# Kernel tuning notes

Measured on AMD Instinct MI355X. Metric: run time of the kernel, lower is better.

## Reference

```python
import jax, jax.numpy as jnp
import numpy as np

N_NODES = 50000
N_EDGES = 800000
D_IN = 64
D_OUT = 64


def setup_inputs() -> dict:
    key = jax.random.key(0)
    ks = jax.random.split(key, 5)
    feat = jax.random.normal(ks[0], (N_NODES, D_IN), dtype=jnp.float32)
    src = jax.random.randint(ks[1], (N_EDGES,), 0, N_NODES, dtype=jnp.int64)
    dst = jax.random.randint(ks[2], (N_EDGES,), 0, N_NODES, dtype=jnp.int64)
    # Xavier-uniform-ish scale for weights
    lim = float(np.sqrt(6.0 / (D_IN + D_OUT)) * np.sqrt(2.0))
    W_neigh = jax.random.uniform(ks[3], (D_OUT, D_IN), dtype=jnp.float32, minval=-lim, maxval=lim)
    W_self = jax.random.uniform(ks[4], (D_OUT, D_IN), dtype=jnp.float32, minval=-lim, maxval=lim)
    b_self = jnp.zeros((D_OUT,), dtype=jnp.float32)
    return {"feat": feat, "src": src, "dst": dst,
            "W_neigh": W_neigh, "W_self": W_self, "b_self": b_self}


def reference(feat, src, dst, W_neigh, W_self, b_self):
    # srcdata = fc_neigh(feat_src)  -> [N, D_OUT]
    srcdata = feat @ W_neigh.T
    # A_div.T @ srcdata == mean of transformed source feats over in-edges per dst.
    # deg[j] = A.sum(0)[j]; column scaling by 1/deg then transpose-SpMM.
    agg = jax.ops.segment_sum(srcdata[src], dst, num_segments=N_NODES)  # [N, D_OUT]
    deg = jax.ops.segment_sum(jnp.ones_like(dst, dtype=srcdata.dtype), dst,
                              num_segments=N_NODES)  # [N]
    # Zero-degree columns stay zero in the sparse product (no stored nonzeros).
    dstdata = jnp.where(deg[:, None] > 0, agg / jnp.maximum(deg, 1.0)[:, None], 0.0)
    # rst = fc_self(feat_dst) + dstdata ; feat_dst = feat[:N_dst] = feat (square A)
    return feat @ W_self.T + b_self + dstdata
```

## Files before the change

kernel.cpp:

```cpp
#include <hip/hip_runtime.h>

#define N_NODES 50000
#define N_EDGES 800000
#define D 64
#define RB 128
#define NBUCK 391
#define NFEATBLK 3125
#define GN 64
#define NCHUNK 196
#define CHUNK 4096
#define SUBCAP 40
#define SCAP 3072
#define ALD 68

typedef __attribute__((ext_vector_type(8))) __bf16 bf16x8;
typedef __attribute__((ext_vector_type(4))) float f32x4;
typedef __attribute__((ext_vector_type(2))) float f32x2;

__device__ inline unsigned f2bf(float f) {
    unsigned b = __builtin_bit_cast(unsigned, f);
    b += 0x7fffu + ((b >> 16) & 1u);
    return b >> 16;
}

__device__ inline void acc16(float* acc, uint4 v) {
    f32x2 a;
    a = __builtin_amdgcn_cvt_pk_f32_fp8((int)v.x, false); acc[0]  += a.x; acc[1]  += a.y;
    a = __builtin_amdgcn_cvt_pk_f32_fp8((int)v.x, true);  acc[2]  += a.x; acc[3]  += a.y;
    a = __builtin_amdgcn_cvt_pk_f32_fp8((int)v.y, false); acc[4]  += a.x; acc[5]  += a.y;
    a = __builtin_amdgcn_cvt_pk_f32_fp8((int)v.y, true);  acc[6]  += a.x; acc[7]  += a.y;
    a = __builtin_amdgcn_cvt_pk_f32_fp8((int)v.z, false); acc[8]  += a.x; acc[9]  += a.y;
    a = __builtin_amdgcn_cvt_pk_f32_fp8((int)v.z, true);  acc[10] += a.x; acc[11] += a.y;
    a = __builtin_amdgcn_cvt_pk_f32_fp8((int)v.w, false); acc[12] += a.x; acc[13] += a.y;
    a = __builtin_amdgcn_cvt_pk_f32_fp8((int)v.w, true);  acc[14] += a.x; acc[15] += a.y;
}

__global__ __launch_bounds__(256) void prep_scatter_kernel(
        const float* __restrict__ feat, const float* __restrict__ Wn, const float* __restrict__ Ws,
        const int* __restrict__ src, const int* __restrict__ dst,
        unsigned* __restrict__ fq,
        unsigned short* __restrict__ wnb, unsigned short* __restrict__ wsb,
        unsigned int* __restrict__ ebuf, unsigned char* __restrict__ cntArr) {
    __shared__ int cntB[NBUCK];
    int b = blockIdx.x;
    int t = threadIdx.x;
    if (b < NCHUNK) {
        for (int i = t; i < NBUCK; i += 256) cntB[i] = 0;
        __syncthreads();
        int e0 = b * CHUNK;
#pragma unroll
        for (int k = 0; k < 16; ++k) {
            int e = e0 + k * 256 + t;
            if (e < N_EDGES) {
                int dv = dst[e];
                int bk = dv >> 7;
                int slot = atomicAdd(&cntB[bk], 1);
                if (slot < SUBCAP)
                    ebuf[((size_t)bk * NCHUNK + b) * SUBCAP + slot] =
                        (unsigned)src[e] | ((unsigned)(dv & (RB - 1)) << 16);
            }
        }
        __syncthreads();
        for (int i = t; i < NBUCK; i += 256) {
            int c = cntB[i];
            cntArr[(size_t)b * NBUCK + i] = (unsigned char)(c < SUBCAP ? c : SUBCAP);
        }
    } else if (b < NCHUNK + NFEATBLK) {
        int i = (b - NCHUNK) * 256 + t;
        float4 v = ((const float4*)feat)[i];
        int q = __builtin_amdgcn_cvt_pk_fp8_f32(v.x, v.y, 0, false);
        q = __builtin_amdgcn_cvt_pk_fp8_f32(v.z, v.w, q, true);
        fq[i] = (unsigned)q;
    } else {
        for (int i = t; i < D * D; i += 256) {
            wnb[i] = (unsigned short)f2bf(Wn[i]);
            wsb[i] = (unsigned short)f2bf(Ws[i]);
        }
    }
}

__global__ __launch_bounds__(256) void gather_mfma_kernel(
        const float* __restrict__ feat, const unsigned char* __restrict__ fq,
        const unsigned int* __restrict__ ebuf, const unsigned char* __restrict__ cntArr,
        const unsigned short* __restrict__ wsb, const unsigned short* __restrict__ wnb,
        const float* __restrict__ bias, float* __restrict__ out) {
    __shared__ int cnt[RB];
    __shared__ int cur[RB];
    __shared__ unsigned short sorted[SCAP];
    __shared__ float agg[GN * ALD];
    int t = threadIdx.x;
    int bk = blockIdx.x >> 1;
    int half = blockIdx.x & 1;
    if (t < RB) cnt[t] = 0;
    __syncthreads();
    int cc = 0;
    const unsigned int* slab = ebuf + ((size_t)bk * NCHUNK + t) * SUBCAP;
    if (t < NCHUNK) cc = cntArr[(size_t)t * NBUCK + bk];
    for (int j = 0; j < cc; j += 4) {
        uint4 v = *(const uint4*)(slab + j);
        atomicAdd(&cnt[(v.x >> 16) & (RB - 1)], 1);
        if (j + 1 < cc) atomicAdd(&cnt[(v.y >> 16) & (RB - 1)], 1);
        if (j + 2 < cc) atomicAdd(&cnt[(v.z >> 16) & (RB - 1)], 1);
        if (j + 3 < cc) atomicAdd(&cnt[(v.w >> 16) & (RB - 1)], 1);
    }
    __syncthreads();
    int c = (t < RB) ? cnt[t] : 0;
    if (t < RB) cur[t] = c;
    __syncthreads();
    for (int d = 1; d < RB; d <<= 1) {
        int v = (t < RB && t >= d) ? cur[t - d] : 0;
        __syncthreads();
        if (t < RB) cur[t] += v;
        __syncthreads();
    }
    if (t < RB) cur[t] -= c;
    __syncthreads();
    for (int j = 0; j < cc; j += 4) {
        uint4 v = *(const uint4*)(slab + j);
        int p;
        p = atomicAdd(&cur[(v.x >> 16) & (RB - 1)], 1);
        if (p < SCAP) sorted[p] = (unsigned short)(v.x & 0xFFFFu);
        if (j + 1 < cc) { p = atomicAdd(&cur[(v.y >> 16) & (RB - 1)], 1); if (p < SCAP) sorted[p] = (unsigned short)(v.y & 0xFFFFu); }
        if (j + 2 < cc) { p = atomicAdd(&cur[(v.z >> 16) & (RB - 1)], 1); if (p < SCAP) sorted[p] = (unsigned short)(v.z & 0xFFFFu); }
        if (j + 3 < cc) { p = atomicAdd(&cur[(v.w >> 16) & (RB - 1)], 1); if (p < SCAP) sorted[p] = (unsigned short)(v.w & 0xFFFFu); }
    }
    __syncthreads();
    int ns = t >> 2, p = t & 3;
    int dl = half * GN + ns;
    int dg = cnt[dl];
    int start = cur[dl] - dg;
    float acc[16];
#pragma unroll
    for (int j = 0; j < 16; ++j) acc[j] = 0.f;
    const unsigned char* fqp = fq + p * 16;
    int i = 0;
    for (; i + 4 <= dg; i += 4) {
        int id0 = sorted[start + i + 0];
        int id1 = sorted[start + i + 1];
        int id2 = sorted[start + i + 2];
        int id3 = sorted[start + i + 3];
        uint4 v0 = *(const uint4*)(fqp + (size_t)id0 * D);
        uint4 v1 = *(const uint4*)(fqp + (size_t)id1 * D);
        uint4 v2 = *(const uint4*)(fqp + (size_t)id2 * D);
        uint4 v3 = *(const uint4*)(fqp + (size_t)id3 * D);
        acc16(acc, v0); acc16(acc, v1); acc16(acc, v2); acc16(acc, v3);
    }
    for (; i < dg; ++i) {
        int id = sorted[start + i];
        uint4 v = *(const uint4*)(fqp + (size_t)id * D);
        acc16(acc, v);
    }
    float inv = (dg > 0) ? 1.0f / (float)dg : 0.f;
#pragma unroll
    for (int j = 0; j < 16; j += 4) {
        float4 o = make_float4(acc[j] * inv, acc[j + 1] * inv, acc[j + 2] * inv, acc[j + 3] * inv);
        *(float4*)(&agg[ns * ALD + p * 16 + j]) = o;
    }
    __syncthreads();
    int r0 = blockIdx.x * GN;
    int w = t >> 6, lane = t & 63;
    int m = lane & 15, quad = lane >> 4;
    int row = r0 + 16 * w + m;
    int rowA = row < N_NODES ? row : N_NODES - 1;
    const float* fr = feat + (size_t)rowA * D + quad * 8;
    float4 f0 = *(const float4*)(fr + 0);
    float4 f1 = *(const float4*)(fr + 4);
    float4 f2 = *(const float4*)(fr + 32);
    float4 f3 = *(const float4*)(fr + 36);
    bf16x8 aS0, aS1, aA0, aA1;
    aS0[0] = (__bf16)f0.x; aS0[1] = (__bf16)f0.y; aS0[2] = (__bf16)f0.z; aS0[3] = (__bf16)f0.w;
    aS0[4] = (__bf16)f1.x; aS0[5] = (__bf16)f1.y; aS0[6] = (__bf16)f1.z; aS0[7] = (__bf16)f1.w;
    aS1[0] = (__bf16)f2.x; aS1[1] = (__bf16)f2.y; aS1[2] = (__bf16)f2.z; aS1[3] = (__bf16)f2.w;
    aS1[4] = (__bf16)f3.x; aS1[5] = (__bf16)f3.y; aS1[6] = (__bf16)f3.z; aS1[7] = (__bf16)f3.w;
#pragma unroll
    for (int j = 0; j < 8; ++j) {
        aA0[j] = (__bf16)agg[(16 * w + m) * ALD + 0  + quad * 8 + j];
        aA1[j] = (__bf16)agg[(16 * w + m) * ALD + 32 + quad * 8 + j];
    }
#pragma unroll
    for (int tt = 0; tt < 4; ++tt) {
        int nn = 16 * tt + m;
        bf16x8 bS0 = *(const bf16x8*)(wsb + (size_t)nn * D + 0  + quad * 8);
        bf16x8 bS1 = *(const bf16x8*)(wsb + (size_t)nn * D + 32 + quad * 8);
        bf16x8 bN0 = *(const bf16x8*)(wnb + (size_t)nn * D + 0  + quad * 8);
        bf16x8 bN1 = *(const bf16x8*)(wnb + (size_t)nn * D + 32 + quad * 8);
        f32x4 cc4 = {0.f, 0.f, 0.f, 0.f};
        cc4 = __builtin_amdgcn_mfma_f32_16x16x32_bf16(aS0, bS0, cc4, 0, 0, 0);
        cc4 = __builtin_amdgcn_mfma_f32_16x16x32_bf16(aS1, bS1, cc4, 0, 0, 0);
        cc4 = __builtin_amdgcn_mfma_f32_16x16x32_bf16(aA0, bN0, cc4, 0, 0, 0);
        cc4 = __builtin_amdgcn_mfma_f32_16x16x32_bf16(aA1, bN1, cc4, 0, 0, 0);
        float bv = bias[16 * tt + m];
#pragma unroll
        for (int reg = 0; reg < 4; ++reg) {
            int orow = r0 + 16 * w + quad * 4 + reg;
            if (orow < N_NODES)
                out[(size_t)orow * D + 16 * tt + m] = cc4[reg] + bv;
        }
    }
}

extern "C" void kernel_launch(void* const* d_in, const int* in_sizes, int n_in,
                              void* d_out, int out_size, void* d_ws, size_t ws_size,
                              hipStream_t stream) {
    const float* feat  = (const float*)d_in[0];
    const int*   src   = (const int*)d_in[1];
    const int*   dst   = (const int*)d_in[2];
    const float* Wn    = (const float*)d_in[3];
    const float* Wself = (const float*)d_in[4];
    const float* bself = (const float*)d_in[5];
    float* out = (float*)d_out;

    unsigned*       featq = (unsigned*)d_ws;
    unsigned short* wnb   = (unsigned short*)(featq + (size_t)N_NODES * D / 4);
    unsigned short* wsb   = wnb + D * D;
    unsigned int*   ebuf  = (unsigned int*)(wsb + D * D);
    unsigned char*  cntArr = (unsigned char*)(ebuf + (size_t)NBUCK * NCHUNK * SUBCAP);

    prep_scatter_kernel<<<NCHUNK + NFEATBLK + 1, 256, 0, stream>>>(
        feat, Wn, Wself, src, dst, featq, wnb, wsb, ebuf, cntArr);
    gather_mfma_kernel<<<2 * NBUCK, 256, 0, stream>>>(
        feat, (const unsigned char*)featq, ebuf, cntArr, wsb, wnb, bself, out);
}
```

Baseline: 113.7 us.

## Replace bucketed LDS counting sort with per-node global atomic edge lists

Edges are no longer binned into 128-node buckets per chunk and then counting-sorted in shared memory. Each edge is now appended straight to a fixed 48-slot list for its destination node in global memory, using global atomics on a per-node counter array that a new init kernel zeroes. The gather kernel then loads each node's ID list with vector loads and skips the LDS histogram, scan and scatter phases. The cost is an extra launch, 800k scattered global atomics, and silent truncation of any node with more than 48 in-edges. The accumulation also switches to packed f32x2 adds.

```diff
diff --git a/kernel.cpp b/kernel.cpp
--- a/kernel.cpp
+++ b/kernel.cpp
@@ -3,14 +3,13 @@
 #define N_NODES 50000
 #define N_EDGES 800000
 #define D 64
-#define RB 128
-#define NBUCK 391
-#define NFEATBLK 3125
 #define GN 64
-#define NCHUNK 196
-#define CHUNK 4096
-#define SUBCAP 40
-#define SCAP 3072
+#define NGB 782
+#define NCAP 48
+#define EPB 1024
+#define NEB 782
+#define NFB 782
+#define SLD 52
 #define ALD 68
 
 typedef __attribute__((ext_vector_type(8))) __bf16 bf16x8;
@@ -23,54 +22,25 @@
     return b >> 16;
 }
 
-__device__ inline void acc16(float* acc, uint4 v) {
-    f32x2 a;
-    a = __builtin_amdgcn_cvt_pk_f32_fp8((int)v.x, false); acc[0]  += a.x; acc[1]  += a.y;
-    a = __builtin_amdgcn_cvt_pk_f32_fp8((int)v.x, true);  acc[2]  += a.x; acc[3]  += a.y;
-    a = __builtin_amdgcn_cvt_pk_f32_fp8((int)v.y, false); acc[4]  += a.x; acc[5]  += a.y;
-    a = __builtin_amdgcn_cvt_pk_f32_fp8((int)v.y, true);  acc[6]  += a.x; acc[7]  += a.y;
-    a = __builtin_amdgcn_cvt_pk_f32_fp8((int)v.z, false); acc[8]  += a.x; acc[9]  += a.y;
-    a = __builtin_amdgcn_cvt_pk_f32_fp8((int)v.z, true);  acc[10] += a.x; acc[11] += a.y;
-    a = __builtin_amdgcn_cvt_pk_f32_fp8((int)v.w, false); acc[12] += a.x; acc[13] += a.y;
-    a = __builtin_amdgcn_cvt_pk_f32_fp8((int)v.w, true);  acc[14] += a.x; acc[15] += a.y;
-}
-
-__global__ __launch_bounds__(256) void prep_scatter_kernel(
-        const float* __restrict__ feat, const float* __restrict__ Wn, const float* __restrict__ Ws,
-        const int* __restrict__ src, const int* __restrict__ dst,
-        unsigned* __restrict__ fq,
-        unsigned short* __restrict__ wnb, unsigned short* __restrict__ wsb,
-        unsigned int* __restrict__ ebuf, unsigned char* __restrict__ cntArr) {
-    __shared__ int cntB[NBUCK];
-    int b = blockIdx.x;
-    int t = threadIdx.x;
-    if (b < NCHUNK) {
-        for (int i = t; i < NBUCK; i += 256) cntB[i] = 0;
-        __syncthreads();
-        int e0 = b * CHUNK;
-#pragma unroll
-        for (int k = 0; k < 16; ++k) {
-            int e = e0 + k * 256 + t;
-            if (e < N_EDGES) {
-                int dv = dst[e];
-                int bk = dv >> 7;
-                int slot = atomicAdd(&cntB[bk], 1);
-                if (slot < SUBCAP)
-                    ebuf[((size_t)bk * NCHUNK + b) * SUBCAP + slot] =
-                        (unsigned)src[e] | ((unsigned)(dv & (RB - 1)) << 16);
-            }
-        }
-        __syncthreads();
-        for (int i = t; i < NBUCK; i += 256) {
-            int c = cntB[i];
-            cntArr[(size_t)b * NBUCK + i] = (unsigned char)(c < SUBCAP ? c : SUBCAP);
-        }
-    } else if (b < NCHUNK + NFEATBLK) {
-        int i = (b - NCHUNK) * 256 + t;
-        float4 v = ((const float4*)feat)[i];
-        int q = __builtin_amdgcn_cvt_pk_fp8_f32(v.x, v.y, 0, false);
-        q = __builtin_amdgcn_cvt_pk_fp8_f32(v.z, v.w, q, true);
-        fq[i] = (unsigned)q;
+__device__ inline void acc16p(f32x2* a, uint4 v) {
+    a[0] += __builtin_amdgcn_cvt_pk_f32_fp8((int)v.x, false);
+    a[1] += __builtin_amdgcn_cvt_pk_f32_fp8((int)v.x, true);
+    a[2] += __builtin_amdgcn_cvt_pk_f32_fp8((int)v.y, false);
+    a[3] += __builtin_amdgcn_cvt_pk_f32_fp8((int)v.y, true);
+    a[4] += __builtin_amdgcn_cvt_pk_f32_fp8((int)v.z, false);
+    a[5] += __builtin_amdgcn_cvt_pk_f32_fp8((int)v.z, true);
+    a[6] += __builtin_amdgcn_cvt_pk_f32_fp8((int)v.w, false);
+    a[7] += __builtin_amdgcn_cvt_pk_f32_fp8((int)v.w, true);
+}
+
+__global__ __launch_bounds__(256) void init_kernel(
+        const float* __restrict__ Wn, const float* __restrict__ Ws,
+        int* __restrict__ cnt,
+        unsigned short* __restrict__ wnb, unsigned short* __restrict__ wsb) {
+    int b = blockIdx.x, t = threadIdx.x;
+    if (b < 49) {
+        int i = b * 256 + t;
+        if (i < N_NODES / 4) ((int4*)cnt)[i] = make_int4(0, 0, 0, 0);
     } else {
         for (int i = t; i < D * D; i += 256) {
             wnb[i] = (unsigned short)f2bf(Wn[i]);
@@ -79,82 +49,92 @@
     }
 }
 
+__global__ __launch_bounds__(256) void prep_kernel(
+        const float* __restrict__ feat,
+        const int* __restrict__ src, const int* __restrict__ dst,
+        unsigned* __restrict__ fq, int* __restrict__ cnt,
+        unsigned* __restrict__ ebuf) {
+    int b = blockIdx.x, t = threadIdx.x;
+    if (b < NEB) {
+        int e0 = b * EPB + t * 4;
+        if (e0 < N_EDGES) {
+            int4 s4 = *(const int4*)(src + e0);
+            int4 d4 = *(const int4*)(dst + e0);
+            int slot;
+            slot = atomicAdd(&cnt[d4.x], 1);
+            if (slot < NCAP) ebuf[(size_t)d4.x * NCAP + slot] = (unsigned)s4.x;
+            slot = atomicAdd(&cnt[d4.y], 1);
+            if (slot < NCAP) ebuf[(size_t)d4.y * NCAP + slot] = (unsigned)s4.y;
+            slot = atomicAdd(&cnt[d4.z], 1);
+            if (slot < NCAP) ebuf[(size_t)d4.z * NCAP + slot] = (unsigned)s4.z;
+            slot = atomicAdd(&cnt[d4.w], 1);
+            if (slot < NCAP) ebuf[(size_t)d4.w * NCAP + slot] = (unsigned)s4.w;
+        }
+    } else {
+        int i0 = (b - NEB) * 1024;
+#pragma unroll
+        for (int k = 0; k < 4; ++k) {
+            int i = i0 + k * 256 + t;
+            if (i < N_NODES * D / 4) {
+                float4 v = ((const float4*)feat)[i];
+                int q = __builtin_amdgcn_cvt_pk_fp8_f32(v.x, v.y, 0, false);
+                q = __builtin_amdgcn_cvt_pk_fp8_f32(v.z, v.w, q, true);
+                fq[i] = (unsigned)q;
+            }
+        }
+    }
+}
+
 __global__ __launch_bounds__(256) void gather_mfma_kernel(
         const float* __restrict__ feat, const unsigned char* __restrict__ fq,
-        const unsigned int* __restrict__ ebuf, const unsigned char* __restrict__ cntArr,
+        const unsigned* __restrict__ ebuf, const int* __restrict__ cnt,
         const unsigned short* __restrict__ wsb, const unsigned short* __restrict__ wnb,
         const float* __restrict__ bias, float* __restrict__ out) {
-    __shared__ int cnt[RB];
-    __shared__ int cur[RB];
-    __shared__ unsigned short sorted[SCAP];
+    __shared__ unsigned sid[GN * SLD];
     __shared__ float agg[GN * ALD];
     int t = threadIdx.x;
-    int bk = blockIdx.x >> 1;
-    int half = blockIdx.x & 1;
-    if (t < RB) cnt[t] = 0;
+    int n0 = blockIdx.x * GN;
+    const uint4* ebase = (const uint4*)(ebuf + (size_t)n0 * NCAP);
+#pragma unroll
+    for (int k = 0; k < 3; ++k) {
+        int wi = k * 256 + t;
+        int node = wi / 12, sub = wi - node * 12;
+        uint4 v = ebase[wi];
+        *(uint4*)(&sid[node * SLD + sub * 4]) = v;
+    }
+    int ns = t >> 2, p = t & 3;
+    int node = n0 + ns;
+    int dg = (node < N_NODES) ? cnt[node] : 0;
+    int dgc = dg < NCAP ? dg : NCAP;
     __syncthreads();
-    int cc = 0;
-    const unsigned int* slab = ebuf + ((size_t)bk * NCHUNK + t) * SUBCAP;
-    if (t < NCHUNK) cc = cntArr[(size_t)t * NBUCK + bk];
-    for (int j = 0; j < cc; j += 4) {
-        uint4 v = *(const uint4*)(slab + j);
-        atomicAdd(&cnt[(v.x >> 16) & (RB - 1)], 1);
-        if (j + 1 < cc) atomicAdd(&cnt[(v.y >> 16) & (RB - 1)], 1);
-        if (j + 2 < cc) atomicAdd(&cnt[(v.z >> 16) & (RB - 1)], 1);
-        if (j + 3 < cc) atomicAdd(&cnt[(v.w >> 16) & (RB - 1)], 1);
-    }
-    __syncthreads();
-    int c = (t < RB) ? cnt[t] : 0;
-    if (t < RB) cur[t] = c;
-    __syncthreads();
-    for (int d = 1; d < RB; d <<= 1) {
-        int v = (t < RB && t >= d) ? cur[t - d] : 0;
-        __syncthreads();
-        if (t < RB) cur[t] += v;
-        __syncthreads();
-    }
-    if (t < RB) cur[t] -= c;
-    __syncthreads();
-    for (int j = 0; j < cc; j += 4) {
-        uint4 v = *(const uint4*)(slab + j);
-        int p;
-        p = atomicAdd(&cur[(v.x >> 16) & (RB - 1)], 1);
-        if (p < SCAP) sorted[p] = (unsigned short)(v.x & 0xFFFFu);
-        if (j + 1 < cc) { p = atomicAdd(&cur[(v.y >> 16) & (RB - 1)], 1); if (p < SCAP) sorted[p] = (unsigned short)(v.y & 0xFFFFu); }
-        if (j + 2 < cc) { p = atomicAdd(&cur[(v.z >> 16) & (RB - 1)], 1); if (p < SCAP) sorted[p] = (unsigned short)(v.z & 0xFFFFu); }
-        if (j + 3 < cc) { p = atomicAdd(&cur[(v.w >> 16) & (RB - 1)], 1); if (p < SCAP) sorted[p] = (unsigned short)(v.w & 0xFFFFu); }
-    }
-    __syncthreads();
-    int ns = t >> 2, p = t & 3;
-    int dl = half * GN + ns;
-    int dg = cnt[dl];
-    int start = cur[dl] - dg;
-    float acc[16];
-#pragma unroll
-    for (int j = 0; j < 16; ++j) acc[j] = 0.f;
+    f32x2 acc2[8];
+#pragma unroll
+    for (int j = 0; j < 8; ++j) acc2[j] = (f32x2){0.f, 0.f};
     const unsigned char* fqp = fq + p * 16;
+    const unsigned* ids = &sid[ns * SLD];
     int i = 0;
-    for (; i + 4 <= dg; i += 4) {
-        int id0 = sorted[start + i + 0];
-        int id1 = sorted[start + i + 1];
-        int id2 = sorted[start + i + 2];
-        int id3 = sorted[start + i + 3];
-        uint4 v0 = *(const uint4*)(fqp + (size_t)id0 * D);
-        uint4 v1 = *(const uint4*)(fqp + (size_t)id1 * D);
-        uint4 v2 = *(const uint4*)(fqp + (size_t)id2 * D);
-        uint4 v3 = *(const uint4*)(fqp + (size_t)id3 * D);
-        acc16(acc, v0); acc16(acc, v1); acc16(acc, v2); acc16(acc, v3);
-    }
-    for (; i < dg; ++i) {
-        int id = sorted[start + i];
-        uint4 v = *(const uint4*)(fqp + (size_t)id * D);
-        acc16(acc, v);
+    for (; i + 4 <= dgc; i += 4) {
+        uint4 id4 = *(const uint4*)(ids + i);
+        uint4 v0 = *(const uint4*)(fqp + (size_t)id4.x * D);
+        uint4 v1 = *(const uint4*)(fqp + (size_t)id4.y * D);
+        uint4 v2 = *(const uint4*)(fqp + (size_t)id4.z * D);
+        uint4 v3 = *(const uint4*)(fqp + (size_t)id4.w * D);
+        acc16p(acc2, v0); acc16p(acc2, v1); acc16p(acc2, v2); acc16p(acc2, v3);
+    }
+    if (i < dgc) {
+        uint4 id4 = *(const uint4*)(ids + i);
+        uint4 v0 = *(const uint4*)(fqp + (size_t)id4.x * D);
+        acc16p(acc2, v0);
+        if (i + 1 < dgc) { uint4 v = *(const uint4*)(fqp + (size_t)id4.y * D); acc16p(acc2, v); }
+        if (i + 2 < dgc) { uint4 v = *(const uint4*)(fqp + (size_t)id4.z * D); acc16p(acc2, v); }
     }
     float inv = (dg > 0) ? 1.0f / (float)dg : 0.f;
-#pragma unroll
-    for (int j = 0; j < 16; j += 4) {
-        float4 o = make_float4(acc[j] * inv, acc[j + 1] * inv, acc[j + 2] * inv, acc[j + 3] * inv);
-        *(float4*)(&agg[ns * ALD + p * 16 + j]) = o;
+    float* ap = &agg[ns * ALD + p * 16];
+#pragma unroll
+    for (int j = 0; j < 4; ++j) {
+        float4 o = make_float4(acc2[2 * j].x * inv, acc2[2 * j].y * inv,
+                               acc2[2 * j + 1].x * inv, acc2[2 * j + 1].y * inv);
+        *(float4*)(ap + 4 * j) = o;
     }
     __syncthreads();
     int r0 = blockIdx.x * GN;
@@ -213,11 +193,11 @@
     unsigned*       featq = (unsigned*)d_ws;
     unsigned short* wnb   = (unsigned short*)(featq + (size_t)N_NODES * D / 4);
     unsigned short* wsb   = wnb + D * D;
-    unsigned int*   ebuf  = (unsigned int*)(wsb + D * D);
-    unsigned char*  cntArr = (unsigned char*)(ebuf + (size_t)NBUCK * NCHUNK * SUBCAP);
-
-    prep_scatter_kernel<<<NCHUNK + NFEATBLK + 1, 256, 0, stream>>>(
-        feat, Wn, Wself, src, dst, featq, wnb, wsb, ebuf, cntArr);
-    gather_mfma_kernel<<<2 * NBUCK, 256, 0, stream>>>(
-        feat, (const unsigned char*)featq, ebuf, cntArr, wsb, wnb, bself, out);
-}
+    int*            cnt   = (int*)(wsb + D * D);
+    unsigned*       ebuf  = (unsigned*)(cnt + N_NODES);
+
+    init_kernel<<<50, 256, 0, stream>>>(Wn, Wself, cnt, wnb, wsb);
+    prep_kernel<<<NEB + NFB, 256, 0, stream>>>(feat, src, dst, featq, cnt, ebuf);
+    gather_mfma_kernel<<<NGB, 256, 0, stream>>>(
+        feat, (const unsigned char*)featq, ebuf, cnt, wsb, wnb, bself, out);
+}
```

Measured after the change: 155.2 us. 1.36x slower.

## Shrink dst buckets to 64 nodes so each gather block sorts only its own rows

Applied to the files above, without the earlier changes.

Destination buckets shrink from 128 to 64 nodes and edge chunks from 4096 to 2048. Each gather block now owns one bucket, so it no longer counts and sorts edges for a twin block's half that it then discards. The prefix scan over bucket counts becomes a wave shuffle scan instead of a barrier-heavy shared-memory scan. FP8 accumulation now uses packed f32x2 adds, and the degree loop is clamped to the sorted-buffer capacity. The tighter SUBCAP and SCAP limits raise the risk of silently dropping edges when a bucket overflows, and there are more chunk slabs to scan per block.

```diff
diff --git a/kernel.cpp b/kernel.cpp
--- a/kernel.cpp
+++ b/kernel.cpp
@@ -3,14 +3,13 @@
 #define N_NODES 50000
 #define N_EDGES 800000
 #define D 64
-#define RB 128
-#define NBUCK 391
+#define RB 64
+#define NBUCK 782
+#define CHUNK 2048
+#define NCHUNK 391
+#define SUBCAP 24
 #define NFEATBLK 3125
-#define GN 64
-#define NCHUNK 196
-#define CHUNK 4096
-#define SUBCAP 40
-#define SCAP 3072
+#define SCAP 1280
 #define ALD 68
 
 typedef __attribute__((ext_vector_type(8))) __bf16 bf16x8;
@@ -23,16 +22,15 @@
     return b >> 16;
 }
 
-__device__ inline void acc16(float* acc, uint4 v) {
-    f32x2 a;
-    a = __builtin_amdgcn_cvt_pk_f32_fp8((int)v.x, false); acc[0]  += a.x; acc[1]  += a.y;
-    a = __builtin_amdgcn_cvt_pk_f32_fp8((int)v.x, true);  acc[2]  += a.x; acc[3]  += a.y;
-    a = __builtin_amdgcn_cvt_pk_f32_fp8((int)v.y, false); acc[4]  += a.x; acc[5]  += a.y;
-    a = __builtin_amdgcn_cvt_pk_f32_fp8((int)v.y, true);  acc[6]  += a.x; acc[7]  += a.y;
-    a = __builtin_amdgcn_cvt_pk_f32_fp8((int)v.z, false); acc[8]  += a.x; acc[9]  += a.y;
-    a = __builtin_amdgcn_cvt_pk_f32_fp8((int)v.z, true);  acc[10] += a.x; acc[11] += a.y;
-    a = __builtin_amdgcn_cvt_pk_f32_fp8((int)v.w, false); acc[12] += a.x; acc[13] += a.y;
-    a = __builtin_amdgcn_cvt_pk_f32_fp8((int)v.w, true);  acc[14] += a.x; acc[15] += a.y;
+__device__ inline void acc16p(f32x2* a, uint4 v) {
+    a[0] += __builtin_amdgcn_cvt_pk_f32_fp8((int)v.x, false);
+    a[1] += __builtin_amdgcn_cvt_pk_f32_fp8((int)v.x, true);
+    a[2] += __builtin_amdgcn_cvt_pk_f32_fp8((int)v.y, false);
+    a[3] += __builtin_amdgcn_cvt_pk_f32_fp8((int)v.y, true);
+    a[4] += __builtin_amdgcn_cvt_pk_f32_fp8((int)v.z, false);
+    a[5] += __builtin_amdgcn_cvt_pk_f32_fp8((int)v.z, true);
+    a[6] += __builtin_amdgcn_cvt_pk_f32_fp8((int)v.w, false);
+    a[7] += __builtin_amdgcn_cvt_pk_f32_fp8((int)v.w, true);
 }
 
 __global__ __launch_bounds__(256) void prep_scatter_kernel(
@@ -49,11 +47,11 @@
         __syncthreads();
         int e0 = b * CHUNK;
 #pragma unroll
-        for (int k = 0; k < 16; ++k) {
+        for (int k = 0; k < 8; ++k) {
             int e = e0 + k * 256 + t;
             if (e < N_EDGES) {
                 int dv = dst[e];
-                int bk = dv >> 7;
+                int bk = dv >> 6;
                 int slot = atomicAdd(&cntB[bk], 1);
                 if (slot < SUBCAP)
                     ebuf[((size_t)bk * NCHUNK + b) * SUBCAP + slot] =
@@ -87,54 +85,59 @@
     __shared__ int cnt[RB];
     __shared__ int cur[RB];
     __shared__ unsigned short sorted[SCAP];
-    __shared__ float agg[GN * ALD];
+    __shared__ float agg[RB * ALD];
     int t = threadIdx.x;
-    int bk = blockIdx.x >> 1;
-    int half = blockIdx.x & 1;
+    int bk = blockIdx.x;
     if (t < RB) cnt[t] = 0;
     __syncthreads();
-    int cc = 0;
-    const unsigned int* slab = ebuf + ((size_t)bk * NCHUNK + t) * SUBCAP;
-    if (t < NCHUNK) cc = cntArr[(size_t)t * NBUCK + bk];
-    for (int j = 0; j < cc; j += 4) {
-        uint4 v = *(const uint4*)(slab + j);
-        atomicAdd(&cnt[(v.x >> 16) & (RB - 1)], 1);
-        if (j + 1 < cc) atomicAdd(&cnt[(v.y >> 16) & (RB - 1)], 1);
-        if (j + 2 < cc) atomicAdd(&cnt[(v.z >> 16) & (RB - 1)], 1);
-        if (j + 3 < cc) atomicAdd(&cnt[(v.w >> 16) & (RB - 1)], 1);
-    }
-    __syncthreads();
-    int c = (t < RB) ? cnt[t] : 0;
-    if (t < RB) cur[t] = c;
-    __syncthreads();
-    for (int d = 1; d < RB; d <<= 1) {
-        int v = (t < RB && t >= d) ? cur[t - d] : 0;
-        __syncthreads();
-        if (t < RB) cur[t] += v;
-        __syncthreads();
-    }
-    if (t < RB) cur[t] -= c;
-    __syncthreads();
-    for (int j = 0; j < cc; j += 4) {
-        uint4 v = *(const uint4*)(slab + j);
-        int p;
-        p = atomicAdd(&cur[(v.x >> 16) & (RB - 1)], 1);
-        if (p < SCAP) sorted[p] = (unsigned short)(v.x & 0xFFFFu);
-        if (j + 1 < cc) { p = atomicAdd(&cur[(v.y >> 16) & (RB - 1)], 1); if (p < SCAP) sorted[p] = (unsigned short)(v.y & 0xFFFFu); }
-        if (j + 2 < cc) { p = atomicAdd(&cur[(v.z >> 16) & (RB - 1)], 1); if (p < SCAP) sorted[p] = (unsigned short)(v.z & 0xFFFFu); }
-        if (j + 3 < cc) { p = atomicAdd(&cur[(v.w >> 16) & (RB - 1)], 1); if (p < SCAP) sorted[p] = (unsigned short)(v.w & 0xFFFFu); }
+    for (int c = t; c < NCHUNK; c += 256) {
+        int cc = cntArr[(size_t)c * NBUCK + bk];
+        const unsigned int* slab = ebuf + ((size_t)bk * NCHUNK + c) * SUBCAP;
+        for (int j = 0; j < cc; j += 4) {
+            uint4 v = *(const uint4*)(slab + j);
+            atomicAdd(&cnt[(v.x >> 16) & (RB - 1)], 1);
+            if (j + 1 < cc) atomicAdd(&cnt[(v.y >> 16) & (RB - 1)], 1);
+            if (j + 2 < cc) atomicAdd(&cnt[(v.z >> 16) & (RB - 1)], 1);
+            if (j + 3 < cc) atomicAdd(&cnt[(v.w >> 16) & (RB - 1)], 1);
+        }
+    }
+    __syncthreads();
+    if (t < RB) {
+        int c = cnt[t];
+        int s = c;
+#pragma unroll
+        for (int d = 1; d < RB; d <<= 1) {
+            int v = __shfl_up(s, d, 64);
+            if (t >= d) s += v;
+        }
+        cur[t] = s - c;
+    }
+    __syncthreads();
+    for (int c = t; c < NCHUNK; c += 256) {
+        int cc = cntArr[(size_t)c * NBUCK + bk];
+        const unsigned int* slab = ebuf + ((size_t)bk * NCHUNK + c) * SUBCAP;
+        for (int j = 0; j < cc; j += 4) {
+            uint4 v = *(const uint4*)(slab + j);
+            int p;
+            p = atomicAdd(&cur[(v.x >> 16) & (RB - 1)], 1);
+            if (p < SCAP) sorted[p] = (unsigned short)(v.x & 0xFFFFu);
+            if (j + 1 < cc) { p = atomicAdd(&cur[(v.y >> 16) & (RB - 1)], 1); if (p < SCAP) sorted[p] = (unsigned short)(v.y & 0xFFFFu); }
+            if (j + 2 < cc) { p = atomicAdd(&cur[(v.z >> 16) & (RB - 1)], 1); if (p < SCAP) sorted[p] = (unsigned short)(v.z & 0xFFFFu); }
+            if (j + 3 < cc) { p = atomicAdd(&cur[(v.w >> 16) & (RB - 1)], 1); if (p < SCAP) sorted[p] = (unsigned short)(v.w & 0xFFFFu); }
+        }
     }
     __syncthreads();
     int ns = t >> 2, p = t & 3;
-    int dl = half * GN + ns;
-    int dg = cnt[dl];
-    int start = cur[dl] - dg;
-    float acc[16];
-#pragma unroll
-    for (int j = 0; j < 16; ++j) acc[j] = 0.f;
+    int dg = cnt[ns];
+    int start = cur[ns] - dg;
+    int dgc = dg;
+    if (start + dgc > SCAP) dgc = (start < SCAP) ? (SCAP - start) : 0;
+    f32x2 acc2[8];
+#pragma unroll
+    for (int j = 0; j < 8; ++j) acc2[j] = (f32x2){0.f, 0.f};
     const unsigned char* fqp = fq + p * 16;
     int i = 0;
-    for (; i + 4 <= dg; i += 4) {
+    for (; i + 4 <= dgc; i += 4) {
         int id0 = sorted[start + i + 0];
         int id1 = sorted[start + i + 1];
         int id2 = sorted[start + i + 2];
@@ -143,21 +146,23 @@
         uint4 v1 = *(const uint4*)(fqp + (size_t)id1 * D);
         uint4 v2 = *(const uint4*)(fqp + (size_t)id2 * D);
         uint4 v3 = *(const uint4*)(fqp + (size_t)id3 * D);
-        acc16(acc, v0); acc16(acc, v1); acc16(acc, v2); acc16(acc, v3);
-    }
-    for (; i < dg; ++i) {
+        acc16p(acc2, v0); acc16p(acc2, v1); acc16p(acc2, v2); acc16p(acc2, v3);
+    }
+    for (; i < dgc; ++i) {
         int id = sorted[start + i];
         uint4 v = *(const uint4*)(fqp + (size_t)id * D);
-        acc16(acc, v);
+        acc16p(acc2, v);
     }
     float inv = (dg > 0) ? 1.0f / (float)dg : 0.f;
-#pragma unroll
-    for (int j = 0; j < 16; j += 4) {
-        float4 o = make_float4(acc[j] * inv, acc[j + 1] * inv, acc[j + 2] * inv, acc[j + 3] * inv);
-        *(float4*)(&agg[ns * ALD + p * 16 + j]) = o;
-    }
-    __syncthreads();
-    int r0 = blockIdx.x * GN;
+    float* ap = &agg[ns * ALD + p * 16];
+#pragma unroll
+    for (int j = 0; j < 4; ++j) {
+        float4 o = make_float4(acc2[2 * j].x * inv, acc2[2 * j].y * inv,
+                               acc2[2 * j + 1].x * inv, acc2[2 * j + 1].y * inv);
+        *(float4*)(ap + 4 * j) = o;
+    }
+    __syncthreads();
+    int r0 = blockIdx.x * RB;
     int w = t >> 6, lane = t & 63;
     int m = lane & 15, quad = lane >> 4;
     int row = r0 + 16 * w + m;
@@ -218,6 +223,6 @@
 
     prep_scatter_kernel<<<NCHUNK + NFEATBLK + 1, 256, 0, stream>>>(
         feat, Wn, Wself, src, dst, featq, wnb, wsb, ebuf, cntArr);
-    gather_mfma_kernel<<<2 * NBUCK, 256, 0, stream>>>(
+    gather_mfma_kernel<<<NBUCK, 256, 0, stream>>>(
         feat, (const unsigned char*)featq, ebuf, cntArr, wsb, wnb, bself, out);
 }
```

Result: no change. 113.8 us (+0.1%).
